# Kernel tuning notes

Hardware: AMD Instinct MI355X
Metric: run time of the kernel (lower is better)

Reference implementation:

```python
import jax, jax.numpy as jnp
import numpy as np

B, S, F, H, O = 256, 512, 64, 1024, 24  # batch, seq_len, input_size, hidden_size, output_size


def setup_inputs() -> dict:
    key = jax.random.key(0)
    ks = jax.random.split(key, 11)
    s = 1.0 / np.sqrt(H)  # PyTorch LSTM/Linear uniform init bound
    u = lambda k, shape: jax.random.uniform(k, shape, jnp.float32, -s, s)
    return {
        "x": jax.random.normal(ks[0], (B, S, F), jnp.float32),
        # layer 0 (gate order: i, f, g, o stacked along first dim)
        "W_ih0": u(ks[1], (4 * H, F)),
        "W_hh0": u(ks[2], (4 * H, H)),
        "b_ih0": u(ks[3], (4 * H,)),
        "b_hh0": u(ks[4], (4 * H,)),
        # layer 1
        "W_ih1": u(ks[5], (4 * H, H)),
        "W_hh1": u(ks[6], (4 * H, H)),
        "b_ih1": u(ks[7], (4 * H,)),
        "b_hh1": u(ks[8], (4 * H,)),
        # final projection over all timesteps: [O, H*S]
        "fc_W": jax.random.uniform(ks[9], (O, H * S), jnp.float32, -1.0 / np.sqrt(H * S), 1.0 / np.sqrt(H * S)),
        "fc_b": jax.random.uniform(ks[10], (O,), jnp.float32, -1.0 / np.sqrt(H * S), 1.0 / np.sqrt(H * S)),
    }


def _lstm_layer(x_sbf, W_ih, W_hh, b_ih, b_hh):
    # x_sbf: [S, B, Fin]; returns all hidden states [S, B, H]
    Hh = W_hh.shape[1]
    # precompute input contribution for all steps (one big GEMM)
    xg = jnp.einsum('sbf,gf->sbg', x_sbf, W_ih) + b_ih + b_hh  # [S, B, 4H]

    def step(carry, xg_t):
        h, c = carry
        gates = xg_t + h @ W_hh.T  # [B, 4H]
        i, f, g, o = jnp.split(gates, 4, axis=-1)
        c = jax.nn.sigmoid(f) * c + jax.nn.sigmoid(i) * jnp.tanh(g)
        h = jax.nn.sigmoid(o) * jnp.tanh(c)
        return (h, c), h

    h0 = jnp.zeros((x_sbf.shape[1], Hh), x_sbf.dtype)
    _, hs = jax.lax.scan(step, (h0, h0), xg)
    return hs  # [S, B, H]


def reference(x, W_ih0, W_hh0, b_ih0, b_hh0, W_ih1, W_hh1, b_ih1, b_hh1, fc_W, fc_b):
    xs = jnp.swapaxes(x, 0, 1)  # [S, B, F]
    h1 = _lstm_layer(xs, W_ih0, W_hh0, b_ih0, b_hh0)  # [S, B, H]
    h2 = _lstm_layer(h1, W_ih1, W_hh1, b_ih1, b_hh1)  # [S, B, H]
    # use_all_h=True: reshape [B, S, H] -> [B, S*H], then Linear
    flat = jnp.swapaxes(h2, 0, 1).reshape(x.shape[0], -1)
    return flat @ fc_W.T + fc_b  # [B, O]
```

## Files before the change

### kernel.cpp

```cpp
#include <hip/hip_runtime.h>
#include <hip/hip_fp16.h>

#define B_ 256
#define S_ 512
#define F_ 64
#define H_ 1024
#define O_ 24
#define G_ 4096
#define NT_ 64

typedef _Float16 half_t;
typedef _Float16 h8 __attribute__((ext_vector_type(8)));
typedef float f4 __attribute__((ext_vector_type(4)));

#define OFF_H1 ((size_t)0)
#define OFF_H2 (OFF_H1 + (size_t)2*B_*H_*2)
#define OFF_C1 (OFF_H2 + (size_t)2*B_*H_*2)
#define OFF_C2 (OFF_C1 + (size_t)B_*H_*4)
#define OFF_OP (OFF_C2 + (size_t)B_*H_*4)
#define ZBYTES (OFF_OP + (size_t)NT_*B_*O_*4)
#define OFF_BIAS0 (ZBYTES)
#define OFF_BIAS1 (OFF_BIAS0 + (size_t)G_*4)
#define OFF_XH    (OFF_BIAS1 + (size_t)G_*4)
#define OFF_WIH0  (OFF_XH + (size_t)B_*S_*F_*2)
#define OFF_WHH0  (OFF_WIH0 + (size_t)G_*F_*2)
#define OFF_WIH1  (OFF_WHH0 + (size_t)G_*H_*2)
#define OFF_WHH1  (OFF_WIH1 + (size_t)G_*H_*2)
#define WS_NEEDED (OFF_WHH1 + (size_t)G_*H_*2)

__global__ void k_bias(const float* __restrict__ bi0, const float* __restrict__ bh0,
                       const float* __restrict__ bi1, const float* __restrict__ bh1,
                       float* __restrict__ bias0, float* __restrict__ bias1) {
    int i = blockIdx.x * blockDim.x + threadIdx.x;
    if (i < G_) { bias0[i] = bi0[i] + bh0[i]; bias1[i] = bi1[i] + bh1[i]; }
}

__global__ void k_cvt(const float* __restrict__ src, half_t* __restrict__ dst, int n) {
    int i = blockIdx.x * blockDim.x + threadIdx.x;
    int stride = gridDim.x * blockDim.x;
    for (; i < n; i += stride) dst[i] = (half_t)src[i];
}

__global__ void k_pack(const float* __restrict__ src, half_t* __restrict__ dst, int NC) {
    int i = blockIdx.x * blockDim.x + threadIdx.x;
    int total = 32768 * NC;
    if (i >= total) return;
    int lane = i & 63;
    int j    = (i >> 6) & 3;
    int ck   = (i >> 8) % NC;
    int gh   = i / (256 * NC);
    int srow = (gh >> 5) * H_ + (gh & 31) * 32 + (j >> 1) * 16 + (lane & 15);
    int scol = ck * 64 + (j & 1) * 32 + (lane >> 4) * 8;
    const float* s = src + (size_t)srow * (NC * 64) + scol;
    h8 v;
    #pragma unroll
    for (int e = 0; e < 8; ++e) v[e] = (half_t)s[e];
    *(h8*)&dst[(size_t)i * 8] = v;
}

__device__ __forceinline__ void run_part(
    const int thr, const int bt, const int htp,
    const int cx, const int nchunks,
    const half_t* __restrict__ xb, const int ldx,
    const half_t* __restrict__ hp,
    const half_t* __restrict__ Wih, const half_t* __restrict__ Whh,
    const float* __restrict__ bias,
    float* __restrict__ c, half_t* __restrict__ hn_out,
    const float* __restrict__ fcWt, float* __restrict__ out_part,
    half_t* A_s, float* gate_s, float* h_s, float* fcw_s,
    const bool do_fc)
{
    const int wave = thr >> 6, lane = thr & 63;
    const int gate = wave >> 1, mh = wave & 1;
    const int quad = lane >> 4, l15 = lane & 15;
    const int ar = thr >> 3;
    const int ak = (thr & 7) * 8;
    const int ghW = gate * 32 + (htp >> 1);
    const int jo  = (htp & 1) * 2;

    float bv = bias[gate * H_ + htp * 16 + l15];
    f4 acc0 = (f4){bv, bv, bv, bv};
    f4 acc1 = acc0;

    auto loadA = [&](int ck) -> f4 {
        const half_t* Ab; int lda, k0;
        if (ck < cx) { Ab = xb; lda = ldx; k0 = ck * 64; }
        else         { Ab = hp; lda = H_;  k0 = (ck - cx) * 64; }
        return *(const f4*)&Ab[(size_t)(bt * 64 + ar) * lda + k0 + ak];
    };
    auto fetchW = [&](int ck, h8& r0, h8& r1) {
        const half_t* Wb; int ckk, NC;
        if (ck < cx) { Wb = Wih; ckk = ck;      NC = cx; }
        else         { Wb = Whh; ckk = ck - cx; NC = 16; }
        const half_t* base = Wb + ((size_t)(((ghW * NC) + ckk) * 4 + jo) * 64 + lane) * 8;
        r0 = *(const h8*)(base + 0 * 512);
        r1 = *(const h8*)(base + 1 * 512);
    };

    h8 Ws0a,Ws0b, Ws1a,Ws1b, Ws2a,Ws2b, Ws3a,Ws3b,
       Ws4a,Ws4b, Ws5a,Ws5b, Ws6a,Ws6b, Ws7a{},Ws7b{};
    f4 p0, p1, p2, p3;
    f4 q0, q1, q2, q3;

    f4 a0_ = loadA(0), a1_ = loadA(1), a2_ = loadA(2), a3_ = loadA(3);
    p0 = loadA(4); p1 = loadA(5); p2 = loadA(6); p3 = loadA(7);
    fetchW(0, Ws0a, Ws0b);
    fetchW(1, Ws1a, Ws1b);
    fetchW(2, Ws2a, Ws2b);
    fetchW(3, Ws3a, Ws3b);
    fetchW(4, Ws4a, Ws4b);
    fetchW(5, Ws5a, Ws5b);
    fetchW(6, Ws6a, Ws6b);

    const int eb = thr >> 4, ecol = thr & 15;
    const size_t cbase = (size_t)(bt * 64 + eb) * H_ + htp * 16 + ecol;
    float cpre0 = c[cbase];
    float cpre1 = c[cbase + (size_t)32 * H_];
    float fpre = 0.f;
    if (do_fc && thr < 384)
        fpre = fcWt[(size_t)(thr >> 4) * (S_ * H_) + htp * 16 + (thr & 15)];

    *(f4*)&A_s[0 * 4608 + ar * 72 + ak] = a0_;
    *(f4*)&A_s[1 * 4608 + ar * 72 + ak] = a1_;
    *(f4*)&A_s[2 * 4608 + ar * 72 + ak] = a2_;
    *(f4*)&A_s[3 * 4608 + ar * 72 + ak] = a3_;
    __syncthreads();

    for (int s = 0; s < nchunks; s += 8) {
        if (s + 8  < nchunks) q0 = loadA(s + 8);
        if (s + 9  < nchunks) q1 = loadA(s + 9);
        if (s + 10 < nchunks) q2 = loadA(s + 10);
        if (s + 11 < nchunks) q3 = loadA(s + 11);

        #define STEP(i, C0,C1, N0,N1)                                                            \
        if (s + i < nchunks) {                                                                   \
            if (s + i + 7 < nchunks) fetchW(s + i + 7, N0, N1);                                  \
            const int bo = (i) < 4 ? 0 : 18432;                                                  \
            const int ii = (i) & 3;                                                              \
            h8 a0 = *(const h8*)&A_s[bo + ii * 4608 + (mh * 32 + l15) * 72 + quad * 8];          \
            h8 a1 = *(const h8*)&A_s[bo + ii * 4608 + (mh * 32 + 16 + l15) * 72 + quad * 8];     \
            h8 a2 = *(const h8*)&A_s[bo + ii * 4608 + (mh * 32 + l15) * 72 + 32 + quad * 8];     \
            h8 a3 = *(const h8*)&A_s[bo + ii * 4608 + (mh * 32 + 16 + l15) * 72 + 32 + quad * 8];\
            acc0 = __builtin_amdgcn_mfma_f32_16x16x32_f16(a0, C0, acc0, 0, 0, 0);                \
            acc1 = __builtin_amdgcn_mfma_f32_16x16x32_f16(a1, C0, acc1, 0, 0, 0);                \
            acc0 = __builtin_amdgcn_mfma_f32_16x16x32_f16(a2, C1, acc0, 0, 0, 0);                \
            acc1 = __builtin_amdgcn_mfma_f32_16x16x32_f16(a3, C1, acc1, 0, 0, 0);                \
        }
        STEP(0, Ws0a,Ws0b, Ws7a,Ws7b)
        STEP(1, Ws1a,Ws1b, Ws0a,Ws0b)
        STEP(2, Ws2a,Ws2b, Ws1a,Ws1b)
        STEP(3, Ws3a,Ws3b, Ws2a,Ws2b)

        if (s + 4 < nchunks) *(f4*)&A_s[18432 + 0 * 4608 + ar * 72 + ak] = p0;
        if (s + 5 < nchunks) *(f4*)&A_s[18432 + 1 * 4608 + ar * 72 + ak] = p1;
        if (s + 6 < nchunks) *(f4*)&A_s[18432 + 2 * 4608 + ar * 72 + ak] = p2;
        if (s + 7 < nchunks) *(f4*)&A_s[18432 + 3 * 4608 + ar * 72 + ak] = p3;

        if (s + 12 < nchunks) p0 = loadA(s + 12);
        if (s + 13 < nchunks) p1 = loadA(s + 13);
        if (s + 14 < nchunks) p2 = loadA(s + 14);
        if (s + 15 < nchunks) p3 = loadA(s + 15);

        __syncthreads();

        STEP(4, Ws4a,Ws4b, Ws3a,Ws3b)
        STEP(5, Ws5a,Ws5b, Ws4a,Ws4b)
        STEP(6, Ws6a,Ws6b, Ws5a,Ws5b)
        STEP(7, Ws7a,Ws7b, Ws6a,Ws6b)
        #undef STEP

        if (s + 8  < nchunks) *(f4*)&A_s[0 * 4608 + ar * 72 + ak] = q0;
        if (s + 9  < nchunks) *(f4*)&A_s[1 * 4608 + ar * 72 + ak] = q1;
        if (s + 10 < nchunks) *(f4*)&A_s[2 * 4608 + ar * 72 + ak] = q2;
        if (s + 11 < nchunks) *(f4*)&A_s[3 * 4608 + ar * 72 + ak] = q3;
        __syncthreads();
    }

    #pragma unroll
    for (int r = 0; r < 4; ++r) {
        gate_s[gate * (64 * 17) + (mh * 32 + quad * 4 + r) * 17 + l15]      = acc0[r];
        gate_s[gate * (64 * 17) + (mh * 32 + 16 + quad * 4 + r) * 17 + l15] = acc1[r];
    }
    __syncthreads();

    #pragma unroll
    for (int kk = 0; kk < 2; ++kk) {
        int b = eb + kk * 32;
        float gi = gate_s[0 * (64 * 17) + b * 17 + ecol];
        float gf = gate_s[1 * (64 * 17) + b * 17 + ecol];
        float gg = gate_s[2 * (64 * 17) + b * 17 + ecol];
        float go = gate_s[3 * (64 * 17) + b * 17 + ecol];
        float si = 1.f / (1.f + __expf(-gi));
        float sf = 1.f / (1.f + __expf(-gf));
        float so = 1.f / (1.f + __expf(-go));
        float tg = tanhf(gg);
        float cn = sf * (kk ? cpre1 : cpre0) + si * tg;
        size_t cidx = cbase + (size_t)kk * 32 * H_;
        c[cidx] = cn;
        float hnv = so * tanhf(cn);
        hn_out[cidx] = (half_t)hnv;
        if (do_fc) h_s[b * 17 + ecol] = hnv;
    }

    if (do_fc) {
        if (thr < 384) fcw_s[thr] = fpre;
        __syncthreads();
        #pragma unroll
        for (int q = 0; q < 3; ++q) {
            int p = thr + q * 512;
            int o = p >> 6, bb = p & 63;
            float s2 = 0.f;
            #pragma unroll
            for (int j = 0; j < 16; ++j)
                s2 += h_s[bb * 17 + j] * fcw_s[o * 16 + j];
            out_part[(size_t)htp * (B_ * O_) + (bt * 64 + bb) * O_ + o] += s2;
        }
    }
    __syncthreads();
}

__global__ __launch_bounds__(512, 2)
void k_phase(int t,
             const half_t* __restrict__ x_h,
             const half_t* __restrict__ Wih0, const half_t* __restrict__ Whh0,
             const float* __restrict__ bias0, float* __restrict__ c1g, half_t* __restrict__ h1buf,
             const half_t* __restrict__ Wih1, const half_t* __restrict__ Whh1,
             const float* __restrict__ bias1, float* __restrict__ c2g, half_t* __restrict__ h2buf,
             const float* __restrict__ fcW, float* __restrict__ out_part)
{
    __shared__ __align__(16) char smraw[73728];
    half_t* A_s    = (half_t*)smraw;
    float*  gate_s = (float*)smraw;
    float*  h_s    = (float*)(smraw + 17408);
    float*  fcw_s  = (float*)(smraw + 21760);

    const int n   = blockIdx.x;
    const int htp = (n & 7) + 8 * ((n >> 3) & 7);
    const int bt  = (n >> 6) & 3;
    const int thr = threadIdx.x;

    if (t < S_) {
        const int tt = t;
        run_part(thr, bt, htp, 1, 17,
                 x_h + (size_t)tt * F_, S_ * F_,
                 h1buf + (size_t)((tt - 1) & 1) * B_ * H_,
                 Wih0, Whh0, bias0, c1g,
                 h1buf + (size_t)(tt & 1) * B_ * H_,
                 nullptr, nullptr,
                 A_s, gate_s, h_s, fcw_s, false);
    }
    if (t > 0) {
        const int tt = t - 1;
        run_part(thr, bt, htp, 16, 32,
                 h1buf + (size_t)(tt & 1) * B_ * H_, H_,
                 h2buf + (size_t)((tt - 1) & 1) * B_ * H_,
                 Wih1, Whh1, bias1, c2g,
                 h2buf + (size_t)(tt & 1) * B_ * H_,
                 fcW + (size_t)tt * H_, out_part,
                 A_s, gate_s, h_s, fcw_s, true);
    }
}

__global__ void k_final(const float* __restrict__ out_part, const float* __restrict__ fcb,
                        float* __restrict__ out) {
    int i = blockIdx.x * blockDim.x + threadIdx.x;
    if (i >= B_ * O_) return;
    int o = i % O_;
    float s = fcb[o];
    for (int tl = 0; tl < NT_; ++tl) s += out_part[(size_t)tl * (B_ * O_) + i];
    out[i] = s;
}

extern "C" void kernel_launch(void* const* d_in, const int* in_sizes, int n_in,
                              void* d_out, int out_size, void* d_ws, size_t ws_size,
                              hipStream_t stream) {
    const float* x    = (const float*)d_in[0];
    const float* Wih0 = (const float*)d_in[1];
    const float* Whh0 = (const float*)d_in[2];
    const float* bih0 = (const float*)d_in[3];
    const float* bhh0 = (const float*)d_in[4];
    const float* Wih1 = (const float*)d_in[5];
    const float* Whh1 = (const float*)d_in[6];
    const float* bih1 = (const float*)d_in[7];
    const float* bhh1 = (const float*)d_in[8];
    const float* fcW  = (const float*)d_in[9];
    const float* fcb  = (const float*)d_in[10];

    char* ws = (char*)d_ws;
    half_t* h1buf  = (half_t*)(ws + OFF_H1);
    half_t* h2buf  = (half_t*)(ws + OFF_H2);
    float*  c1     = (float*)(ws + OFF_C1);
    float*  c2     = (float*)(ws + OFF_C2);
    float*  opart  = (float*)(ws + OFF_OP);
    float*  bias0  = (float*)(ws + OFF_BIAS0);
    float*  bias1  = (float*)(ws + OFF_BIAS1);
    half_t* x_h    = (half_t*)(ws + OFF_XH);
    half_t* wih0_p = (half_t*)(ws + OFF_WIH0);
    half_t* whh0_p = (half_t*)(ws + OFF_WHH0);
    half_t* wih1_p = (half_t*)(ws + OFF_WIH1);
    half_t* whh1_p = (half_t*)(ws + OFF_WHH1);

    hipMemsetAsync(d_ws, 0, ZBYTES, stream);

    k_bias<<<dim3((G_ + 255) / 256), dim3(256), 0, stream>>>(bih0, bhh0, bih1, bhh1, bias0, bias1);
    k_cvt<<<dim3(2048), dim3(256), 0, stream>>>(x, x_h, B_ * S_ * F_);
    k_pack<<<dim3(128),  dim3(256), 0, stream>>>(Wih0, wih0_p, 1);
    k_pack<<<dim3(2048), dim3(256), 0, stream>>>(Whh0, whh0_p, 16);
    k_pack<<<dim3(2048), dim3(256), 0, stream>>>(Wih1, wih1_p, 16);
    k_pack<<<dim3(2048), dim3(256), 0, stream>>>(Whh1, whh1_p, 16);

    dim3 grid(256), blk(512);
    for (int t = 0; t <= S_; ++t) {
        k_phase<<<grid, blk, 0, stream>>>(t, x_h,
                                          wih0_p, whh0_p, bias0, c1, h1buf,
                                          wih1_p, whh1_p, bias1, c2, h2buf,
                                          fcW, opart);
    }
    k_final<<<dim3((B_ * O_ + 255) / 256), dim3(256), 0, stream>>>(opart, fcb, (float*)d_out);
}
```

Measured before the change: 10.26 ms.

## Split K across wave pairs instead of M, halving per-wave weight register footprint

Each pair of waves per gate now splits the K chunks (even/odd) and covers all 64 batch rows, instead of splitting the rows. Each wave therefore fetches only half the weight chunks and needs a shallower register prefetch ring (4 slots instead of 8), and the two partial sums are reduced through LDS at the end. Block barriers are replaced with a barrier that waits only on LDS counters, so outstanding global loads are not drained at each sync. The trade-off is more LDS A-fragment reads per wave, an extra reduction pass, and the reliance on the LDS-only wait being sufficient for correctness.

```diff
diff --git a/kernel.cpp b/kernel.cpp
--- a/kernel.cpp
+++ b/kernel.cpp
@@ -58,6 +58,12 @@
     *(h8*)&dst[(size_t)i * 8] = v;
 }
 
+
+__device__ __forceinline__ void bar_lds() {
+    asm volatile("s_waitcnt lgkmcnt(0)" ::: "memory");
+    __builtin_amdgcn_s_barrier();
+}
+
 __device__ __forceinline__ void run_part(
     const int thr, const int bt, const int htp,
     const int cx, const int nchunks,
@@ -71,16 +77,18 @@
     const bool do_fc)
 {
     const int wave = thr >> 6, lane = thr & 63;
-    const int gate = wave >> 1, mh = wave & 1;
+    const int gate = wave >> 1, kh = wave & 1;
     const int quad = lane >> 4, l15 = lane & 15;
     const int ar = thr >> 3;
     const int ak = (thr & 7) * 8;
     const int ghW = gate * 32 + (htp >> 1);
     const int jo  = (htp & 1) * 2;
 
-    float bv = bias[gate * H_ + htp * 16 + l15];
+    float bv = (kh == 0) ? bias[gate * H_ + htp * 16 + l15] : 0.f;
     f4 acc0 = (f4){bv, bv, bv, bv};
     f4 acc1 = acc0;
+    f4 acc2 = acc0;
+    f4 acc3 = acc0;
 
     auto loadA = [&](int ck) -> f4 {
         const half_t* Ab; int lda, k0;
@@ -97,20 +105,14 @@
         r1 = *(const h8*)(base + 1 * 512);
     };
 
-    h8 Ws0a,Ws0b, Ws1a,Ws1b, Ws2a,Ws2b, Ws3a,Ws3b,
-       Ws4a,Ws4b, Ws5a,Ws5b, Ws6a,Ws6b, Ws7a{},Ws7b{};
+    h8 W0a,W0b, W1a,W1b, W2a,W2b, W3a,W3b;
     f4 p0, p1, p2, p3;
     f4 q0, q1, q2, q3;
-
     f4 a0_ = loadA(0), a1_ = loadA(1), a2_ = loadA(2), a3_ = loadA(3);
     p0 = loadA(4); p1 = loadA(5); p2 = loadA(6); p3 = loadA(7);
-    fetchW(0, Ws0a, Ws0b);
-    fetchW(1, Ws1a, Ws1b);
-    fetchW(2, Ws2a, Ws2b);
-    fetchW(3, Ws3a, Ws3b);
-    fetchW(4, Ws4a, Ws4b);
-    fetchW(5, Ws5a, Ws5b);
-    fetchW(6, Ws6a, Ws6b);
+    fetchW(kh,     W0a, W0b);
+    fetchW(kh + 2, W1a, W1b);
+    fetchW(kh + 4, W2a, W2b);
 
     const int eb = thr >> 4, ecol = thr & 15;
     const size_t cbase = (size_t)(bt * 64 + eb) * H_ + htp * 16 + ecol;
@@ -124,7 +126,31 @@
     *(f4*)&A_s[1 * 4608 + ar * 72 + ak] = a1_;
     *(f4*)&A_s[2 * 4608 + ar * 72 + ak] = a2_;
     *(f4*)&A_s[3 * 4608 + ar * 72 + ak] = a3_;
-    __syncthreads();
+    bar_lds();
+
+    #define STEP(coff, BUFO, C0, C1, N0, N1)                                               \
+    {   const int cc = s + (coff) + kh;                                                    \
+        if (cc < nchunks) {                                                                \
+            if (cc + 6 < nchunks) fetchW(cc + 6, N0, N1);                                  \
+            const int ao = (BUFO) + (((coff) + kh) & 3) * 4608;                            \
+            h8 a00 = *(const h8*)&A_s[ao + (0  + l15) * 72 + quad * 8];                    \
+            h8 a10 = *(const h8*)&A_s[ao + (16 + l15) * 72 + quad * 8];                    \
+            h8 a20 = *(const h8*)&A_s[ao + (32 + l15) * 72 + quad * 8];                    \
+            h8 a30 = *(const h8*)&A_s[ao + (48 + l15) * 72 + quad * 8];                    \
+            h8 a01 = *(const h8*)&A_s[ao + (0  + l15) * 72 + 32 + quad * 8];               \
+            h8 a11 = *(const h8*)&A_s[ao + (16 + l15) * 72 + 32 + quad * 8];               \
+            h8 a21 = *(const h8*)&A_s[ao + (32 + l15) * 72 + 32 + quad * 8];               \
+            h8 a31 = *(const h8*)&A_s[ao + (48 + l15) * 72 + 32 + quad * 8];               \
+            acc0 = __builtin_amdgcn_mfma_f32_16x16x32_f16(a00, C0, acc0, 0, 0, 0);         \
+            acc1 = __builtin_amdgcn_mfma_f32_16x16x32_f16(a10, C0, acc1, 0, 0, 0);         \
+            acc2 = __builtin_amdgcn_mfma_f32_16x16x32_f16(a20, C0, acc2, 0, 0, 0);         \
+            acc3 = __builtin_amdgcn_mfma_f32_16x16x32_f16(a30, C0, acc3, 0, 0, 0);         \
+            acc0 = __builtin_amdgcn_mfma_f32_16x16x32_f16(a01, C1, acc0, 0, 0, 0);         \
+            acc1 = __builtin_amdgcn_mfma_f32_16x16x32_f16(a11, C1, acc1, 0, 0, 0);         \
+            acc2 = __builtin_amdgcn_mfma_f32_16x16x32_f16(a21, C1, acc2, 0, 0, 0);         \
+            acc3 = __builtin_amdgcn_mfma_f32_16x16x32_f16(a31, C1, acc3, 0, 0, 0);         \
+        }                                                                                  \
+    }
 
     for (int s = 0; s < nchunks; s += 8) {
         if (s + 8  < nchunks) q0 = loadA(s + 8);
@@ -132,24 +158,8 @@
         if (s + 10 < nchunks) q2 = loadA(s + 10);
         if (s + 11 < nchunks) q3 = loadA(s + 11);
 
-        #define STEP(i, C0,C1, N0,N1)                                                            \
-        if (s + i < nchunks) {                                                                   \
-            if (s + i + 7 < nchunks) fetchW(s + i + 7, N0, N1);                                  \
-            const int bo = (i) < 4 ? 0 : 18432;                                                  \
-            const int ii = (i) & 3;                                                              \
-            h8 a0 = *(const h8*)&A_s[bo + ii * 4608 + (mh * 32 + l15) * 72 + quad * 8];          \
-            h8 a1 = *(const h8*)&A_s[bo + ii * 4608 + (mh * 32 + 16 + l15) * 72 + quad * 8];     \
-            h8 a2 = *(const h8*)&A_s[bo + ii * 4608 + (mh * 32 + l15) * 72 + 32 + quad * 8];     \
-            h8 a3 = *(const h8*)&A_s[bo + ii * 4608 + (mh * 32 + 16 + l15) * 72 + 32 + quad * 8];\
-            acc0 = __builtin_amdgcn_mfma_f32_16x16x32_f16(a0, C0, acc0, 0, 0, 0);                \
-            acc1 = __builtin_amdgcn_mfma_f32_16x16x32_f16(a1, C0, acc1, 0, 0, 0);                \
-            acc0 = __builtin_amdgcn_mfma_f32_16x16x32_f16(a2, C1, acc0, 0, 0, 0);                \
-            acc1 = __builtin_amdgcn_mfma_f32_16x16x32_f16(a3, C1, acc1, 0, 0, 0);                \
-        }
-        STEP(0, Ws0a,Ws0b, Ws7a,Ws7b)
-        STEP(1, Ws1a,Ws1b, Ws0a,Ws0b)
-        STEP(2, Ws2a,Ws2b, Ws1a,Ws1b)
-        STEP(3, Ws3a,Ws3b, Ws2a,Ws2b)
+        STEP(0, 0,     W0a,W0b, W3a,W3b)
+        STEP(2, 0,     W1a,W1b, W0a,W0b)
 
         if (s + 4 < nchunks) *(f4*)&A_s[18432 + 0 * 4608 + ar * 72 + ak] = p0;
         if (s + 5 < nchunks) *(f4*)&A_s[18432 + 1 * 4608 + ar * 72 + ak] = p1;
@@ -161,27 +171,39 @@
         if (s + 14 < nchunks) p2 = loadA(s + 14);
         if (s + 15 < nchunks) p3 = loadA(s + 15);
 
-        __syncthreads();
-
-        STEP(4, Ws4a,Ws4b, Ws3a,Ws3b)
-        STEP(5, Ws5a,Ws5b, Ws4a,Ws4b)
-        STEP(6, Ws6a,Ws6b, Ws5a,Ws5b)
-        STEP(7, Ws7a,Ws7b, Ws6a,Ws6b)
-        #undef STEP
+        bar_lds();
+
+        STEP(4, 18432, W2a,W2b, W1a,W1b)
+        STEP(6, 18432, W3a,W3b, W2a,W2b)
 
         if (s + 8  < nchunks) *(f4*)&A_s[0 * 4608 + ar * 72 + ak] = q0;
         if (s + 9  < nchunks) *(f4*)&A_s[1 * 4608 + ar * 72 + ak] = q1;
         if (s + 10 < nchunks) *(f4*)&A_s[2 * 4608 + ar * 72 + ak] = q2;
         if (s + 11 < nchunks) *(f4*)&A_s[3 * 4608 + ar * 72 + ak] = q3;
-        __syncthreads();
-    }
-
-    #pragma unroll
-    for (int r = 0; r < 4; ++r) {
-        gate_s[gate * (64 * 17) + (mh * 32 + quad * 4 + r) * 17 + l15]      = acc0[r];
-        gate_s[gate * (64 * 17) + (mh * 32 + 16 + quad * 4 + r) * 17 + l15] = acc1[r];
-    }
-    __syncthreads();
+        bar_lds();
+    }
+    #undef STEP
+
+    if (kh == 0) {
+        #pragma unroll
+        for (int r = 0; r < 4; ++r) {
+            gate_s[gate * (64 * 17) + (0  + quad * 4 + r) * 17 + l15] = acc0[r];
+            gate_s[gate * (64 * 17) + (16 + quad * 4 + r) * 17 + l15] = acc1[r];
+            gate_s[gate * (64 * 17) + (32 + quad * 4 + r) * 17 + l15] = acc2[r];
+            gate_s[gate * (64 * 17) + (48 + quad * 4 + r) * 17 + l15] = acc3[r];
+        }
+    }
+    bar_lds();
+    if (kh == 1) {
+        #pragma unroll
+        for (int r = 0; r < 4; ++r) {
+            gate_s[gate * (64 * 17) + (0  + quad * 4 + r) * 17 + l15] += acc0[r];
+            gate_s[gate * (64 * 17) + (16 + quad * 4 + r) * 17 + l15] += acc1[r];
+            gate_s[gate * (64 * 17) + (32 + quad * 4 + r) * 17 + l15] += acc2[r];
+            gate_s[gate * (64 * 17) + (48 + quad * 4 + r) * 17 + l15] += acc3[r];
+        }
+    }
+    bar_lds();
 
     #pragma unroll
     for (int kk = 0; kk < 2; ++kk) {
@@ -204,7 +226,7 @@
 
     if (do_fc) {
         if (thr < 384) fcw_s[thr] = fpre;
-        __syncthreads();
+        bar_lds();
         #pragma unroll
         for (int q = 0; q < 3; ++q) {
             int p = thr + q * 512;
@@ -216,7 +238,7 @@
             out_part[(size_t)htp * (B_ * O_) + (bt * 64 + bb) * O_ + o] += s2;
         }
     }
-    __syncthreads();
+    bar_lds();
 }
 
 __global__ __launch_bounds__(512, 2)
```

After: 9.803 ms. 1.05x faster.
